# Performance work log

Hardware: AMD Instinct MI355X
Metric: run time of the kernel (lower is better)

Reference implementation:

```python
import jax, jax.numpy as jnp
import numpy as np

H = 128  # LSTM units

def setup_inputs() -> dict:
    key = jax.random.key(0)
    ks = jax.random.split(key, 4)
    B, T, F = 16384, 28, 28
    x = jax.random.normal(ks[0], (B, T, F), dtype=jnp.float32)
    W = jax.random.normal(ks[1], (F, 4 * H), dtype=jnp.float32) * (1.0 / np.sqrt(F))
    U = jax.random.normal(ks[2], (H, 4 * H), dtype=jnp.float32) * (1.0 / np.sqrt(H))
    b = jnp.zeros((4 * H,), dtype=jnp.float32)
    Wd = jax.random.normal(ks[3], (H, 10), dtype=jnp.float32) * (1.0 / np.sqrt(H))
    bd = jnp.zeros((10,), dtype=jnp.float32)
    return {"x": x, "W": W, "U": U, "b": b, "Wd": Wd, "bd": bd}

def reference(x, W, U, b, Wd, bd):
    B = x.shape[0]
    # Precompute input projection for all timesteps: [B, T, 4H]
    xW = jnp.einsum('btf,fg->btg', x, W) + b
    xW_t = jnp.swapaxes(xW, 0, 1)  # [T, B, 4H] for scan

    def step(carry, xw):
        h, c = carry
        z = xw + h @ U  # [B, 4H]
        i, f, g, o = jnp.split(z, 4, axis=-1)  # Keras gate order: i, f, c, o
        i = jax.nn.sigmoid(i)
        f = jax.nn.sigmoid(f)
        g = jax.nn.relu(g)          # activation='relu' on cell candidate
        o = jax.nn.sigmoid(o)
        c_new = f * c + i * g
        h_new = o * jax.nn.relu(c_new)  # activation='relu' on cell state
        return (h_new, c_new), None

    h0 = jnp.zeros((B, H), dtype=x.dtype)
    c0 = jnp.zeros((B, H), dtype=x.dtype)
    (h_final, _), _ = jax.lax.scan(step, (h0, c0), xW_t)
    logits = h_final @ Wd + bd
    return jax.nn.softmax(logits, axis=-1)
```

## Files before the change

### kernel.cpp

```cpp
#include <hip/hip_runtime.h>
#include <math.h>

constexpr int LH = 128;
constexpr int LG = 512;
constexpr int LT = 28;
constexpr int LF = 28;
constexpr int NS = 16;
constexpr int NTH = 512;
constexpr int NREC = 8 * 4 * 5;

typedef short bf16x8 __attribute__((ext_vector_type(8)));
typedef float f32x4  __attribute__((ext_vector_type(4)));

__device__ __forceinline__ unsigned short rne_bf16(float f) {
    unsigned u = __builtin_bit_cast(unsigned, f);
    u += 0x7FFFu + ((u >> 16) & 1u);
    return (unsigned short)(u >> 16);
}
__device__ __forceinline__ float bf16_to_f(unsigned short v) {
    return __builtin_bit_cast(float, (unsigned)v << 16);
}
__device__ __forceinline__ float fsigmoid(float v) {
    return __builtin_amdgcn_rcpf(1.0f + __expf(-v));
}

__device__ __forceinline__ int h_idx(int row, int g, int w2) {
    return row * LH + (((g ^ (row & 15)) << 3) + w2);
}

__global__ __launch_bounds__(256) void pack_frags(
    const float* __restrict__ W, const float* __restrict__ U,
    const float* __restrict__ b, unsigned short* __restrict__ ws)
{
    const int gid = blockIdx.x * 256 + threadIdx.x;
    if (gid >= NREC * 64) return;
    const int lane = gid & 63;
    const int rec  = gid >> 6;
    const int kk   = rec % 5;
    const int wti  = rec / 5;
    const int ti   = wti & 3;
    const int w    = wti >> 2;
    const int r16  = lane & 15;
    const int quad = lane >> 4;
    const int col  = 128 * ti + 16 * w + r16;

    unsigned short v[8];
#pragma unroll
    for (int e = 0; e < 8; ++e) {
        float f;
        if (kk < 4) {
            f = U[(kk * 32 + quad * 8 + e) * LG + col];
        } else {
            const int k = quad * 8 + e;
            f = (k < LF) ? W[k * LG + col] : (k == LF ? b[col] : 0.0f);
        }
        v[e] = rne_bf16(f);
    }
    unsigned short* dst = ws + (size_t)gid * 8;
#pragma unroll
    for (int e = 0; e < 8; ++e) dst[e] = v[e];
}

__global__ __launch_bounds__(NTH, 4) void lstm_mfma(
    const float* __restrict__ x,
    const bf16x8* __restrict__ frag,
    const float* __restrict__ Wd,
    const float* __restrict__ bd,
    float* __restrict__ out)
{
    __shared__ unsigned short xfrag[LT][4][16][8];
    __shared__ unsigned short h_sh[2][NS * LH];
    __shared__ bf16x8 wlds[8 * 4 * 64];
    __shared__ float logit_lds[NS][10];

    const int tid  = threadIdx.x;
    const int wave = tid >> 6;
    const int lane = tid & 63;
    const int r16  = lane & 15;
    const int quad = lane >> 4;
    const long s0  = (long)blockIdx.x * NS;

    bf16x8 Uf[4][4];
#pragma unroll
    for (int ti = 0; ti < 4; ++ti)
#pragma unroll
        for (int kk = 0; kk < 4; ++kk)
            Uf[ti][kk] = frag[((wave * 4 + ti) * 5 + kk) * 64 + lane];

    for (int i = tid; i < 8 * 4 * 64; i += NTH)
        wlds[i] = frag[((i >> 6) * 5 + 4) * 64 + (i & 63)];

    for (int i = tid; i < NS * LH; i += NTH) h_sh[0][i] = 0;

#pragma unroll 1
    for (int i = tid; i < LT * NS * 32; i += NTH) {
        const int fpad = i & 31;
        const int s    = (i >> 5) & 15;
        const int t    = i >> 9;
        float v;
        if (fpad < LF)       v = x[(s0 + s) * (LT * LF) + t * LF + fpad];
        else if (fpad == LF) v = 1.0f;
        else                 v = 0.0f;
        xfrag[t][fpad >> 3][s][fpad & 7] = rne_bf16(v);
    }

    float cre[4];
#pragma unroll
    for (int e = 0; e < 4; ++e) cre[e] = 0.0f;

    int cur = 0;
#pragma unroll 1
    for (int t = 0; t < LT; ++t) {
        __syncthreads();

        f32x4 acc[4];
#pragma unroll
        for (int ti = 0; ti < 4; ++ti)
            acc[ti] = f32x4{0.0f, 0.0f, 0.0f, 0.0f};

        {
            const bf16x8 xa = *reinterpret_cast<const bf16x8*>(
                &xfrag[t][quad][r16][0]);
#pragma unroll
            for (int ti = 0; ti < 4; ++ti) {
                const bf16x8 wf = wlds[(wave * 4 + ti) * 64 + lane];
                acc[ti] = __builtin_amdgcn_mfma_f32_16x16x32_bf16(
                    xa, wf, acc[ti], 0, 0, 0);
            }
        }

#pragma unroll
        for (int kk = 0; kk < 4; ++kk) {
            const bf16x8 h0 = *reinterpret_cast<const bf16x8*>(
                &h_sh[cur][h_idx(r16, kk * 4 + quad, 0)]);
#pragma unroll
            for (int ti = 0; ti < 4; ++ti)
                acc[ti] = __builtin_amdgcn_mfma_f32_16x16x32_bf16(
                    h0, Uf[ti][kk], acc[ti], 0, 0, 0);
        }

        const int gW = 2 * wave + (r16 >> 3);
        const int w2 = r16 & 7;
#pragma unroll
        for (int e = 0; e < 4; ++e) {
            const float ig = fsigmoid(acc[0][e]);
            const float fg = fsigmoid(acc[1][e]);
            const float gg = fmaxf(acc[2][e], 0.0f);
            const float og = fsigmoid(acc[3][e]);
            const float cn = fg * cre[e] + ig * gg;
            cre[e] = cn;
            const float hv = og * fmaxf(cn, 0.0f);
            h_sh[cur ^ 1][h_idx(quad * 4 + e, gW, w2)] = rne_bf16(hv);
        }
        cur ^= 1;
    }

    __syncthreads();

    if (tid < NS * 10) {
        const int s   = tid / 10;
        const int cls = tid - s * 10;
        float a = bd[cls];
        for (int k = 0; k < LH; ++k) {
            const float hv = bf16_to_f(
                h_sh[cur][s * LH + ((((k >> 3) ^ s) << 3) + (k & 7))]);
            a += hv * Wd[k * 10 + cls];
        }
        logit_lds[s][cls] = a;
    }
    __syncthreads();

    if (tid < NS) {
        const int s = tid;
        float m = logit_lds[s][0];
#pragma unroll
        for (int q = 1; q < 10; ++q) m = fmaxf(m, logit_lds[s][q]);
        float e[10], sum = 0.0f;
#pragma unroll
        for (int q = 0; q < 10; ++q) {
            e[q] = expf(logit_lds[s][q] - m);
            sum += e[q];
        }
        const float inv = __builtin_amdgcn_rcpf(sum);
#pragma unroll
        for (int q = 0; q < 10; ++q)
            out[(s0 + s) * 10 + q] = e[q] * inv;
    }
}

extern "C" void kernel_launch(void* const* d_in, const int* in_sizes, int n_in,
                              void* d_out, int out_size, void* d_ws, size_t ws_size,
                              hipStream_t stream) {
    const float* x  = (const float*)d_in[0];
    const float* W  = (const float*)d_in[1];
    const float* U  = (const float*)d_in[2];
    const float* b  = (const float*)d_in[3];
    const float* Wd = (const float*)d_in[4];
    const float* bd = (const float*)d_in[5];
    float* out = (float*)d_out;

    const int B = in_sizes[0] / (LT * LF);
    const int blocks = B / NS;

    pack_frags<<<(NREC * 64 + 255) / 256, 256, 0, stream>>>(
        W, U, b, (unsigned short*)d_ws);
    lstm_mfma<<<blocks, NTH, 0, stream>>>(
        x, (const bf16x8*)d_ws, Wd, bd, out);
}
```

Measured before the change: 108.3 us.

## Read input-projection fragments from global per step, reorder MFMAs, add setprio

New measurement: 106.9 us. Within noise of the previous version (-1.3%).

```diff
diff --git a/kernel.cpp b/kernel.cpp
--- a/kernel.cpp
+++ b/kernel.cpp
@@ -1,4 +1,5 @@
 #include <hip/hip_runtime.h>
+#include <hip/hip_bf16.h>
 #include <math.h>
 
 constexpr int LH = 128;
@@ -16,6 +17,10 @@
     unsigned u = __builtin_bit_cast(unsigned, f);
     u += 0x7FFFu + ((u >> 16) & 1u);
     return (unsigned short)(u >> 16);
+}
+__device__ __forceinline__ unsigned short hw_bf16(float f) {
+    __hip_bfloat16 h = __float2bfloat16(f);
+    return __builtin_bit_cast(unsigned short, h);
 }
 __device__ __forceinline__ float bf16_to_f(unsigned short v) {
     return __builtin_bit_cast(float, (unsigned)v << 16);
@@ -70,7 +75,6 @@
 {
     __shared__ unsigned short xfrag[LT][4][16][8];
     __shared__ unsigned short h_sh[2][NS * LH];
-    __shared__ bf16x8 wlds[8 * 4 * 64];
     __shared__ float logit_lds[NS][10];
 
     const int tid  = threadIdx.x;
@@ -87,8 +91,10 @@
         for (int kk = 0; kk < 4; ++kk)
             Uf[ti][kk] = frag[((wave * 4 + ti) * 5 + kk) * 64 + lane];
 
-    for (int i = tid; i < 8 * 4 * 64; i += NTH)
-        wlds[i] = frag[((i >> 6) * 5 + 4) * 64 + (i & 63)];
+    const bf16x8* wrec0 = &frag[((wave * 4 + 0) * 5 + 4) * 64 + lane];
+    const bf16x8* wrec1 = &frag[((wave * 4 + 1) * 5 + 4) * 64 + lane];
+    const bf16x8* wrec2 = &frag[((wave * 4 + 2) * 5 + 4) * 64 + lane];
+    const bf16x8* wrec3 = &frag[((wave * 4 + 3) * 5 + 4) * 64 + lane];
 
     for (int i = tid; i < NS * LH; i += NTH) h_sh[0][i] = 0;
 
@@ -113,22 +119,20 @@
     for (int t = 0; t < LT; ++t) {
         __syncthreads();
 
+        const bf16x8 wf0 = *wrec0;
+        const bf16x8 wf1 = *wrec1;
+        const bf16x8 wf2 = *wrec2;
+        const bf16x8 wf3 = *wrec3;
+
         f32x4 acc[4];
 #pragma unroll
         for (int ti = 0; ti < 4; ++ti)
             acc[ti] = f32x4{0.0f, 0.0f, 0.0f, 0.0f};
 
-        {
-            const bf16x8 xa = *reinterpret_cast<const bf16x8*>(
-                &xfrag[t][quad][r16][0]);
-#pragma unroll
-            for (int ti = 0; ti < 4; ++ti) {
-                const bf16x8 wf = wlds[(wave * 4 + ti) * 64 + lane];
-                acc[ti] = __builtin_amdgcn_mfma_f32_16x16x32_bf16(
-                    xa, wf, acc[ti], 0, 0, 0);
-            }
-        }
-
+        const bf16x8 xa = *reinterpret_cast<const bf16x8*>(
+            &xfrag[t][quad][r16][0]);
+
+        __builtin_amdgcn_s_setprio(1);
 #pragma unroll
         for (int kk = 0; kk < 4; ++kk) {
             const bf16x8 h0 = *reinterpret_cast<const bf16x8*>(
@@ -138,6 +142,11 @@
                 acc[ti] = __builtin_amdgcn_mfma_f32_16x16x32_bf16(
                     h0, Uf[ti][kk], acc[ti], 0, 0, 0);
         }
+        acc[0] = __builtin_amdgcn_mfma_f32_16x16x32_bf16(xa, wf0, acc[0], 0, 0, 0);
+        acc[1] = __builtin_amdgcn_mfma_f32_16x16x32_bf16(xa, wf1, acc[1], 0, 0, 0);
+        acc[2] = __builtin_amdgcn_mfma_f32_16x16x32_bf16(xa, wf2, acc[2], 0, 0, 0);
+        acc[3] = __builtin_amdgcn_mfma_f32_16x16x32_bf16(xa, wf3, acc[3], 0, 0, 0);
+        __builtin_amdgcn_s_setprio(0);
 
         const int gW = 2 * wave + (r16 >> 3);
         const int w2 = r16 & 7;
@@ -150,7 +159,7 @@
             const float cn = fg * cre[e] + ig * gg;
             cre[e] = cn;
             const float hv = og * fmaxf(cn, 0.0f);
-            h_sh[cur ^ 1][h_idx(quad * 4 + e, gW, w2)] = rne_bf16(hv);
+            h_sh[cur ^ 1][h_idx(quad * 4 + e, gW, w2)] = hw_bf16(hv);
         }
         cur ^= 1;
     }
```
